# Kernel tuning notes

Hardware: AMD Instinct MI355X
Metric: run time of the kernel (lower is better)

Reference implementation:

```python
import jax, jax.numpy as jnp
import numpy as np

N_NODES = 50000
N_EDGES = 800000
D = 128
N_LAYERS = 5
N_REL = 500
N_ENT = 50000  # fc output size (num_entities)
BATCH = 1024


def setup_inputs() -> dict:
    key = jax.random.key(0)
    ks = jax.random.split(key, 10)
    return {
        "entity_embed": jax.random.normal(ks[0], (N_NODES, D), dtype=jnp.float32),
        "edge_val": jnp.ones((N_EDGES,), dtype=jnp.float32),
        "gnn_W": jax.random.normal(ks[1], (N_LAYERS, D, D), dtype=jnp.float32) * (1.0 / np.sqrt(D)),
        "gnn_b": jax.random.normal(ks[2], (N_LAYERS, D), dtype=jnp.float32) * 0.01,
        "rel_table": jax.random.normal(ks[3], (N_REL, D), dtype=jnp.float32),
        "fc_W": jax.random.normal(ks[4], (2 * D, N_ENT), dtype=jnp.float32) * (1.0 / np.sqrt(2 * D)),
        "fc_b": jax.random.normal(ks[5], (N_ENT,), dtype=jnp.float32) * 0.01,
        "edge_row": jax.random.randint(ks[6], (N_EDGES,), 0, N_NODES, dtype=jnp.int32),
        "edge_col": jax.random.randint(ks[7], (N_EDGES,), 0, N_NODES, dtype=jnp.int32),
        "head_idx": jax.random.randint(ks[8], (BATCH,), 0, N_NODES, dtype=jnp.int32),
        "rel_ids": jax.random.randint(ks[9], (BATCH,), 0, N_REL, dtype=jnp.int32),
    }


def reference(entity_embed, edge_val, gnn_W, gnn_b, rel_table, fc_W, fc_b,
              edge_row, edge_col, head_idx, rel_ids):
    n_nodes = entity_embed.shape[0]

    def layer(x, wb):
        W, b = wb
        # sparse.mm(adj, x): out[row] += val * x[col]
        msgs = edge_val[:, None] * x[edge_col]          # [E, D]
        agg = jax.ops.segment_sum(msgs, edge_row, num_segments=n_nodes)  # [N, D]
        return jax.nn.relu(agg @ W + b), None

    all_embed, _ = jax.lax.scan(layer, entity_embed, (gnn_W, gnn_b))

    head_embed = all_embed[head_idx]                    # [B, D]
    rel_embed = rel_table[rel_ids]                      # [B, D]
    embed = jnp.concatenate([head_embed, rel_embed], axis=1)  # [B, 2D]
    logits = embed @ fc_W + fc_b                        # [B, N_ENT]
    return logits
```

## Files before the change

kernel.cpp:

```cpp
#include <hip/hip_runtime.h>


#define N_NODES 50000
#define N_EDGES 800000
#define D 128
#define N_LAYERS 5
#define N_ENT 50000
#define BATCH 1024
#define KDIM 256
#define SCAN_BLOCKS ((N_NODES + 255) / 256)
#define FC_NT 128

typedef __attribute__((ext_vector_type(8))) __bf16 bf16x8;
typedef __attribute__((ext_vector_type(4))) float f32x4;
typedef __attribute__((ext_vector_type(8))) unsigned short u16x8;
typedef __attribute__((ext_vector_type(4))) unsigned short u16x4;

__device__ inline unsigned short f2bf(float x) {
  unsigned int u = __float_as_uint(x);
  unsigned int r = (u + 0x7FFFu + ((u >> 16) & 1u)) >> 16;
  return (unsigned short)r;
}
__device__ inline float bf2f(unsigned short b) {
  return __uint_as_float(((unsigned int)b) << 16);
}

__global__ void zero_i32(int* __restrict__ p, int n) {
  int i = blockIdx.x * blockDim.x + threadIdx.x;
  if (i < n) p[i] = 0;
}

__global__ void hist_kernel(const int* __restrict__ rows, int* __restrict__ counts) {
  int i = blockIdx.x * blockDim.x + threadIdx.x;
  int stride = gridDim.x * blockDim.x;
  for (; i < N_EDGES; i += stride) atomicAdd(&counts[rows[i]], 1);
}

__device__ inline int block_exscan256(int v, int* wsum, int* tot) {
  int t = threadIdx.x, lane = t & 63, wid = t >> 6;
  int s = v;
#pragma unroll
  for (int off = 1; off < 64; off <<= 1) {
    int u = __shfl_up(s, off, 64);
    if (lane >= off) s += u;
  }
  if (lane == 63) wsum[wid] = s;
  __syncthreads();
  if (t == 0) {
    int run = 0;
#pragma unroll
    for (int w = 0; w < 4; ++w) { int tmp = wsum[w]; wsum[w] = run; run += tmp; }
    wsum[4] = run;
  }
  __syncthreads();
  *tot = wsum[4];
  return wsum[wid] + s - v;
}

__global__ __launch_bounds__(256) void scan1_kernel(const int* __restrict__ counts,
                                                    int* __restrict__ row_ptr,
                                                    int* __restrict__ bsum) {
  __shared__ int wsum[5];
  int i = blockIdx.x * 256 + threadIdx.x;
  int v = (i < N_NODES) ? counts[i] : 0;
  int tot;
  int ex = block_exscan256(v, wsum, &tot);
  if (i < N_NODES) row_ptr[i] = ex;
  if (threadIdx.x == 0) bsum[blockIdx.x] = tot;
}

__global__ __launch_bounds__(256) void scan2_kernel(int* __restrict__ bsum) {
  __shared__ int wsum[5];
  int t = threadIdx.x;
  int v = (t < SCAN_BLOCKS) ? bsum[t] : 0;
  int tot;
  int ex = block_exscan256(v, wsum, &tot);
  if (t < SCAN_BLOCKS) bsum[t] = ex;
}

__global__ __launch_bounds__(256) void scan3_kernel(const int* __restrict__ counts,
                                                    const int* __restrict__ bsum,
                                                    int* __restrict__ row_ptr,
                                                    int* __restrict__ cursor) {
  int i = blockIdx.x * 256 + threadIdx.x;
  if (i >= N_NODES) return;
  int ex = row_ptr[i] + bsum[blockIdx.x];
  row_ptr[i] = ex;
  cursor[i] = ex;
  if (i == N_NODES - 1) row_ptr[N_NODES] = ex + counts[i];
}

__global__ void scatter_kernel(const int* __restrict__ rows, const int* __restrict__ cols,
                               const float* __restrict__ vals, int* __restrict__ cursor,
                               int* __restrict__ col_s, float* __restrict__ val_s) {
  int i = blockIdx.x * blockDim.x + threadIdx.x;
  int stride = gridDim.x * blockDim.x;
  for (; i < N_EDGES; i += stride) {
    int r = rows[i];
    int pos = atomicAdd(&cursor[r], 1);
    col_s[pos] = cols[i];
    val_s[pos] = vals[i];
  }
}

__global__ __launch_bounds__(256) void tobf16_kernel(const float* __restrict__ src,
                                                     unsigned short* __restrict__ dst,
                                                     int n8) {
  int i = blockIdx.x * blockDim.x + threadIdx.x;
  if (i >= n8) return;
  float4 a = *(const float4*)&src[i * 8];
  float4 b = *(const float4*)&src[i * 8 + 4];
  u16x8 o;
  o[0] = f2bf(a.x); o[1] = f2bf(a.y); o[2] = f2bf(a.z); o[3] = f2bf(a.w);
  o[4] = f2bf(b.x); o[5] = f2bf(b.y); o[6] = f2bf(b.z); o[7] = f2bf(b.w);
  *(u16x8*)&dst[i * 8] = o;
}

__global__ void wconv_kernel(const float* __restrict__ gW, unsigned short* __restrict__ Wt5) {
  int idx = blockIdx.x * 256 + threadIdx.x;
  if (idx >= N_LAYERS * D * D) return;
  int l = idx / (D * D);
  int rem = idx - l * D * D;
  int j = rem >> 7;
  int k = rem & 127;
  Wt5[idx] = f2bf(gW[l * D * D + k * D + j]);
}

__global__ __launch_bounds__(256) void layer_fused(const unsigned short* __restrict__ xb,
                                                   const int* __restrict__ row_ptr,
                                                   const int* __restrict__ cols,
                                                   const float* __restrict__ vals,
                                                   const unsigned short* __restrict__ Bt,
                                                   const float* __restrict__ bias,
                                                   unsigned short* __restrict__ yb) {
  __shared__ unsigned short atile[64 * D];
  int t = threadIdx.x, lane = t & 63, wave = t >> 6;
  int q = lane >> 4, l16 = lane & 15;
  int r0 = blockIdx.x * 64;
  char* ab = (char*)atile;

#pragma unroll
  for (int p = 0; p < 4; ++p) {
    int row_l = wave * 16 + p * 4 + q;
    int r = r0 + row_l;
    float acc[8] = {0.f, 0.f, 0.f, 0.f, 0.f, 0.f, 0.f, 0.f};
    if (r < N_NODES) {
      int e0 = row_ptr[r], e1 = row_ptr[r + 1];
      for (int base = e0; base < e1; base += 16) {
        int idx = base + l16;
        bool ok = idx < e1;
        int cl = ok ? cols[idx] : 0;
        float vl = ok ? vals[idx] : 0.f;
        int cnt = min(16, e1 - base);
        int j = 0;
        for (; j + 4 <= cnt; j += 4) {
          int c[4]; float v[4]; u16x8 xv[4];
#pragma unroll
          for (int u = 0; u < 4; ++u) {
            c[u] = __shfl(cl, q * 16 + j + u);
            v[u] = __shfl(vl, q * 16 + j + u);
          }
#pragma unroll
          for (int u = 0; u < 4; ++u) xv[u] = *(const u16x8*)&xb[c[u] * D + l16 * 8];
#pragma unroll
          for (int u = 0; u < 4; ++u)
#pragma unroll
            for (int dd = 0; dd < 8; ++dd) acc[dd] = fmaf(v[u], bf2f(xv[u][dd]), acc[dd]);
        }
        for (; j < cnt; ++j) {
          int c = __shfl(cl, q * 16 + j);
          float v = __shfl(vl, q * 16 + j);
          u16x8 xv0 = *(const u16x8*)&xb[c * D + l16 * 8];
#pragma unroll
          for (int dd = 0; dd < 8; ++dd) acc[dd] = fmaf(v, bf2f(xv0[dd]), acc[dd]);
        }
      }
    }
    u16x8 o;
#pragma unroll
    for (int dd = 0; dd < 8; ++dd) o[dd] = f2bf(acc[dd]);
    *(u16x8*)(ab + row_l * 256 + ((l16 ^ (row_l & 7)) << 4)) = o;
  }
  __syncthreads();

  int lq = lane >> 4;
  f32x4 acc2[4][2];
#pragma unroll
  for (int m = 0; m < 4; ++m) { acc2[m][0] = (f32x4){0,0,0,0}; acc2[m][1] = (f32x4){0,0,0,0}; }
#pragma unroll
  for (int kk = 0; kk < 4; ++kk) {
    bf16x8 wfr[2];
#pragma unroll
    for (int nt = 0; nt < 2; ++nt)
      wfr[nt] = *(const bf16x8*)&Bt[(wave * 32 + nt * 16 + l16) * D + kk * 32 + lq * 8];
#pragma unroll
    for (int m = 0; m < 4; ++m) {
      int row_l = m * 16 + l16;
      bf16x8 afr = *(const bf16x8*)(ab + row_l * 256 + ((((kk * 4 + lq) ^ (row_l & 7)) << 4)));
      acc2[m][0] = __builtin_amdgcn_mfma_f32_16x16x32_bf16(wfr[0], afr, acc2[m][0], 0, 0, 0);
      acc2[m][1] = __builtin_amdgcn_mfma_f32_16x16x32_bf16(wfr[1], afr, acc2[m][1], 0, 0, 0);
    }
  }
#pragma unroll
  for (int nt = 0; nt < 2; ++nt) {
    int jb = wave * 32 + nt * 16 + lq * 4;
    float4 bb = *(const float4*)&bias[jb];
#pragma unroll
    for (int m = 0; m < 4; ++m) {
      int r = r0 + m * 16 + l16;
      if (r < N_NODES) {
        u16x4 o;
        o[0] = f2bf(fmaxf(acc2[m][nt][0] + bb.x, 0.f));
        o[1] = f2bf(fmaxf(acc2[m][nt][1] + bb.y, 0.f));
        o[2] = f2bf(fmaxf(acc2[m][nt][2] + bb.z, 0.f));
        o[3] = f2bf(fmaxf(acc2[m][nt][3] + bb.w, 0.f));
        *(u16x4*)&yb[(size_t)r * D + jb] = o;
      }
    }
  }
}

__global__ __launch_bounds__(256) void wt_kernel(const float* __restrict__ fcW,
                                                 unsigned short* __restrict__ Wt) {
  int n = blockIdx.x * 256 + threadIdx.x;
  int k0 = blockIdx.y * 8;
  if (n >= N_ENT) return;
  u16x8 pk;
#pragma unroll
  for (int e = 0; e < 8; ++e) pk[e] = f2bf(fcW[(size_t)(k0 + e) * N_ENT + n]);
  *(u16x8*)&Wt[(size_t)n * KDIM + k0] = pk;
}

__global__ __launch_bounds__(256) void gather_bf16(const unsigned short* __restrict__ xb,
                                                   const float* __restrict__ rel_table,
                                                   const int* __restrict__ head_idx,
                                                   const int* __restrict__ rel_ids,
                                                   unsigned short* __restrict__ ebf) {
  int b = blockIdx.x;
  int k = threadIdx.x;
  unsigned short v;
  if (k < D) v = xb[head_idx[b] * D + k];
  else       v = f2bf(rel_table[rel_ids[b] * D + (k - D)]);
  ebf[b * KDIM + k] = v;
}

__global__ __launch_bounds__(256, 2) void fc_mfma(const unsigned short* __restrict__ ebf,
                                                  const unsigned short* __restrict__ Wt,
                                                  const float* __restrict__ fcb,
                                                  float* __restrict__ out) {
  __shared__ unsigned short etile[64 * KDIM];
  int t = threadIdx.x;
  int lane = t & 63, wave = t >> 6;
  int l16 = lane & 15, lq = lane >> 4;
  int n0 = blockIdx.x * FC_NT;
  char* eb = (char*)etile;

  bf16x8 afr[2][8];
#pragma unroll
  for (int nt = 0; nt < 2; ++nt) {
    const unsigned short* wp = Wt + (size_t)(n0 + wave * 32 + nt * 16 + l16) * KDIM + lq * 8;
#pragma unroll
    for (int kk = 0; kk < 8; ++kk) afr[nt][kk] = *(const bf16x8*)(wp + kk * 32);
  }

  int n_st[2]; float4 bv[2];
#pragma unroll
  for (int nt = 0; nt < 2; ++nt) {
    n_st[nt] = n0 + wave * 32 + nt * 16 + lq * 4;
    bv[nt] = make_float4(0.f, 0.f, 0.f, 0.f);
    if (n_st[nt] < N_ENT) bv[nt] = *(const float4*)&fcb[n_st[nt]];
  }

  for (int bc = 0; bc < 8; ++bc) {
    int b0 = blockIdx.y * 512 + bc * 64;
    const char* esrc = (const char*)(ebf + (size_t)b0 * KDIM);
#pragma unroll
    for (int it = 0; it < 8; ++it) {
      int c = it * 256 + t;
      int row = c >> 5;
      int ci = c & 31;
      float4 v = *(const float4*)(esrc + (size_t)c * 16);
      *(float4*)(eb + row * 512 + ((ci ^ ((row & 7) << 2)) << 4)) = v;
    }
    __syncthreads();

    f32x4 acc[2][4];
#pragma unroll
    for (int nt = 0; nt < 2; ++nt)
#pragma unroll
      for (int m = 0; m < 4; ++m) acc[nt][m] = (f32x4){0.f, 0.f, 0.f, 0.f};

#pragma unroll
    for (int m = 0; m < 4; ++m) {
      int row = m * 16 + l16;
#pragma unroll
      for (int kk = 0; kk < 8; ++kk) {
        bf16x8 bfr = *(const bf16x8*)(eb + row * 512 + ((((kk * 4 + lq) ^ ((row & 7) << 2)) << 4)));
        acc[0][m] = __builtin_amdgcn_mfma_f32_16x16x32_bf16(afr[0][kk], bfr, acc[0][m], 0, 0, 0);
        acc[1][m] = __builtin_amdgcn_mfma_f32_16x16x32_bf16(afr[1][kk], bfr, acc[1][m], 0, 0, 0);
      }
    }

#pragma unroll
    for (int nt = 0; nt < 2; ++nt) {
      if (n_st[nt] < N_ENT) {
#pragma unroll
        for (int m = 0; m < 4; ++m) {
          int b = b0 + m * 16 + l16;
          float4 o = {acc[nt][m][0] + bv[nt].x, acc[nt][m][1] + bv[nt].y,
                      acc[nt][m][2] + bv[nt].z, acc[nt][m][3] + bv[nt].w};
          *(float4*)&out[(size_t)b * N_ENT + n_st[nt]] = o;
        }
      }
    }
    __syncthreads();
  }
}

extern "C" void kernel_launch(void* const* d_in, const int* in_sizes, int n_in,
                              void* d_out, int out_size, void* d_ws, size_t ws_size,
                              hipStream_t stream) {
  const float* entity    = (const float*)d_in[0];
  const float* edge_val  = (const float*)d_in[1];
  const float* gnn_W     = (const float*)d_in[2];
  const float* gnn_b     = (const float*)d_in[3];
  const float* rel_table = (const float*)d_in[4];
  const float* fc_W      = (const float*)d_in[5];
  const float* fc_b      = (const float*)d_in[6];
  const int* edge_row    = (const int*)d_in[7];
  const int* edge_col    = (const int*)d_in[8];
  const int* head_idx    = (const int*)d_in[9];
  const int* rel_ids     = (const int*)d_in[10];
  float* out = (float*)d_out;

  char* ws = (char*)d_ws;
  size_t off = 0;
  auto alloc = [&](size_t bytes) -> void* {
    void* p = ws + off;
    off = (off + bytes + 255) & ~(size_t)255;
    return p;
  };
  int* counts   = (int*)alloc((size_t)N_NODES * 4);
  int* row_ptr  = (int*)alloc((size_t)(N_NODES + 1) * 4);
  int* cursor   = (int*)alloc((size_t)N_NODES * 4);
  int* bsum     = (int*)alloc((size_t)256 * 4);
  int* col_s    = (int*)alloc((size_t)N_EDGES * 4);
  float* val_s  = (float*)alloc((size_t)N_EDGES * 4);
  unsigned short* xA    = (unsigned short*)alloc((size_t)N_NODES * D * 2);
  unsigned short* xB    = (unsigned short*)alloc((size_t)N_NODES * D * 2);
  unsigned short* entbf = (unsigned short*)alloc((size_t)N_NODES * D * 2);
  unsigned short* ebf   = (unsigned short*)alloc((size_t)BATCH * KDIM * 2);
  unsigned short* Wt    = (unsigned short*)alloc((size_t)(N_ENT + 256) * KDIM * 2);
  unsigned short* Wt5   = (unsigned short*)alloc((size_t)N_LAYERS * D * D * 2);

  zero_i32<<<(N_NODES + 255) / 256, 256, 0, stream>>>(counts, N_NODES);
  hist_kernel<<<1024, 256, 0, stream>>>(edge_row, counts);
  scan1_kernel<<<SCAN_BLOCKS, 256, 0, stream>>>(counts, row_ptr, bsum);
  scan2_kernel<<<1, 256, 0, stream>>>(bsum);
  scan3_kernel<<<SCAN_BLOCKS, 256, 0, stream>>>(counts, bsum, row_ptr, cursor);
  scatter_kernel<<<1024, 256, 0, stream>>>(edge_row, edge_col, edge_val, cursor, col_s, val_s);

  tobf16_kernel<<<(N_NODES * D / 8 + 255) / 256, 256, 0, stream>>>(entity, entbf, N_NODES * D / 8);
  wconv_kernel<<<(N_LAYERS * D * D + 255) / 256, 256, 0, stream>>>(gnn_W, Wt5);

  for (int layer = 0; layer < N_LAYERS; ++layer) {
    const unsigned short* xin = (layer == 0) ? entbf : ((layer & 1) ? xA : xB);
    unsigned short* yout = (layer & 1) ? xB : xA;
    layer_fused<<<(N_NODES + 63) / 64, 256, 0, stream>>>(xin, row_ptr, col_s, val_s,
                                                         Wt5 + (size_t)layer * D * D,
                                                         gnn_b + (size_t)layer * D, yout);
  }

  dim3 wtg((N_ENT + 255) / 256, KDIM / 8);
  wt_kernel<<<wtg, 256, 0, stream>>>(fc_W, Wt);
  gather_bf16<<<BATCH, KDIM, 0, stream>>>(xA, rel_table, head_idx, rel_ids, ebf);

  dim3 fcg((N_ENT + FC_NT - 1) / FC_NT, 2);
  fc_mfma<<<fcg, 256, 0, stream>>>(ebf, Wt, fc_b, out);
}
```

Measured before the change: 401.2 us.

## Compute final GNN layer only for the batch's head nodes

The last message-passing layer now runs only on the 1024 head-index rows instead of all 50000 nodes. A new kernel aggregates neighbours and applies W+bias+ReLU for just those rows, writing straight into the FC input buffer. A separate kernel fills the relation half, replacing the old gather kernel. This removes about a fifth of the GNN aggregation work plus one full-graph layer launch. It relies on the output needing only the head rows, which holds for this model.

```diff
diff --git a/kernel.cpp b/kernel.cpp
--- a/kernel.cpp
+++ b/kernel.cpp
@@ -124,6 +124,32 @@
   int j = rem >> 7;
   int k = rem & 127;
   Wt5[idx] = f2bf(gW[l * D * D + k * D + j]);
+}
+
+__device__ inline void agg_batch(int cl, float vl, int cnt, int q, int l16,
+                                 const unsigned short* __restrict__ xb, float* acc) {
+  int j = 0;
+  for (; j + 4 <= cnt; j += 4) {
+    int c[4]; float v[4]; u16x8 xv[4];
+#pragma unroll
+    for (int u = 0; u < 4; ++u) {
+      c[u] = __shfl(cl, q * 16 + j + u);
+      v[u] = __shfl(vl, q * 16 + j + u);
+    }
+#pragma unroll
+    for (int u = 0; u < 4; ++u) xv[u] = *(const u16x8*)&xb[c[u] * D + l16 * 8];
+#pragma unroll
+    for (int u = 0; u < 4; ++u)
+#pragma unroll
+      for (int dd = 0; dd < 8; ++dd) acc[dd] = fmaf(v[u], bf2f(xv[u][dd]), acc[dd]);
+  }
+  for (; j < cnt; ++j) {
+    int c = __shfl(cl, q * 16 + j);
+    float v = __shfl(vl, q * 16 + j);
+    u16x8 xv0 = *(const u16x8*)&xb[c * D + l16 * 8];
+#pragma unroll
+    for (int dd = 0; dd < 8; ++dd) acc[dd] = fmaf(v, bf2f(xv0[dd]), acc[dd]);
+  }
 }
 
 __global__ __launch_bounds__(256) void layer_fused(const unsigned short* __restrict__ xb,
@@ -151,29 +177,7 @@
         bool ok = idx < e1;
         int cl = ok ? cols[idx] : 0;
         float vl = ok ? vals[idx] : 0.f;
-        int cnt = min(16, e1 - base);
-        int j = 0;
-        for (; j + 4 <= cnt; j += 4) {
-          int c[4]; float v[4]; u16x8 xv[4];
-#pragma unroll
-          for (int u = 0; u < 4; ++u) {
-            c[u] = __shfl(cl, q * 16 + j + u);
-            v[u] = __shfl(vl, q * 16 + j + u);
-          }
-#pragma unroll
-          for (int u = 0; u < 4; ++u) xv[u] = *(const u16x8*)&xb[c[u] * D + l16 * 8];
-#pragma unroll
-          for (int u = 0; u < 4; ++u)
-#pragma unroll
-            for (int dd = 0; dd < 8; ++dd) acc[dd] = fmaf(v[u], bf2f(xv[u][dd]), acc[dd]);
-        }
-        for (; j < cnt; ++j) {
-          int c = __shfl(cl, q * 16 + j);
-          float v = __shfl(vl, q * 16 + j);
-          u16x8 xv0 = *(const u16x8*)&xb[c * D + l16 * 8];
-#pragma unroll
-          for (int dd = 0; dd < 8; ++dd) acc[dd] = fmaf(v, bf2f(xv0[dd]), acc[dd]);
-        }
+        agg_batch(cl, vl, min(16, e1 - base), q, l16, xb, acc);
       }
     }
     u16x8 o;
@@ -220,6 +224,84 @@
   }
 }
 
+__global__ __launch_bounds__(256) void layer_head(const unsigned short* __restrict__ xb,
+                                                  const int* __restrict__ row_ptr,
+                                                  const int* __restrict__ cols,
+                                                  const float* __restrict__ vals,
+                                                  const int* __restrict__ head_idx,
+                                                  const unsigned short* __restrict__ Bt,
+                                                  const float* __restrict__ bias,
+                                                  unsigned short* __restrict__ ebf) {
+  __shared__ unsigned short atile[64 * D];
+  int t = threadIdx.x, lane = t & 63, wave = t >> 6;
+  int q = lane >> 4, l16 = lane & 15;
+  int r0 = blockIdx.x * 64;
+  char* ab = (char*)atile;
+
+#pragma unroll
+  for (int p = 0; p < 4; ++p) {
+    int row_l = wave * 16 + p * 4 + q;
+    int b = r0 + row_l;
+    int r = head_idx[b];
+    float acc[8] = {0.f, 0.f, 0.f, 0.f, 0.f, 0.f, 0.f, 0.f};
+    int e0 = row_ptr[r], e1 = row_ptr[r + 1];
+    for (int base = e0; base < e1; base += 16) {
+      int idx = base + l16;
+      bool ok = idx < e1;
+      int cl = ok ? cols[idx] : 0;
+      float vl = ok ? vals[idx] : 0.f;
+      agg_batch(cl, vl, min(16, e1 - base), q, l16, xb, acc);
+    }
+    u16x8 o;
+#pragma unroll
+    for (int dd = 0; dd < 8; ++dd) o[dd] = f2bf(acc[dd]);
+    *(u16x8*)(ab + row_l * 256 + ((l16 ^ (row_l & 7)) << 4)) = o;
+  }
+  __syncthreads();
+
+  int lq = lane >> 4;
+  f32x4 acc2[4][2];
+#pragma unroll
+  for (int m = 0; m < 4; ++m) { acc2[m][0] = (f32x4){0,0,0,0}; acc2[m][1] = (f32x4){0,0,0,0}; }
+#pragma unroll
+  for (int kk = 0; kk < 4; ++kk) {
+    bf16x8 wfr[2];
+#pragma unroll
+    for (int nt = 0; nt < 2; ++nt)
+      wfr[nt] = *(const bf16x8*)&Bt[(wave * 32 + nt * 16 + l16) * D + kk * 32 + lq * 8];
+#pragma unroll
+    for (int m = 0; m < 4; ++m) {
+      int row_l = m * 16 + l16;
+      bf16x8 afr = *(const bf16x8*)(ab + row_l * 256 + ((((kk * 4 + lq) ^ (row_l & 7)) << 4)));
+      acc2[m][0] = __builtin_amdgcn_mfma_f32_16x16x32_bf16(wfr[0], afr, acc2[m][0], 0, 0, 0);
+      acc2[m][1] = __builtin_amdgcn_mfma_f32_16x16x32_bf16(wfr[1], afr, acc2[m][1], 0, 0, 0);
+    }
+  }
+#pragma unroll
+  for (int nt = 0; nt < 2; ++nt) {
+    int jb = wave * 32 + nt * 16 + lq * 4;
+    float4 bb = *(const float4*)&bias[jb];
+#pragma unroll
+    for (int m = 0; m < 4; ++m) {
+      int b = r0 + m * 16 + l16;
+      u16x4 o;
+      o[0] = f2bf(fmaxf(acc2[m][nt][0] + bb.x, 0.f));
+      o[1] = f2bf(fmaxf(acc2[m][nt][1] + bb.y, 0.f));
+      o[2] = f2bf(fmaxf(acc2[m][nt][2] + bb.z, 0.f));
+      o[3] = f2bf(fmaxf(acc2[m][nt][3] + bb.w, 0.f));
+      *(u16x4*)&ebf[(size_t)b * KDIM + jb] = o;
+    }
+  }
+}
+
+__global__ __launch_bounds__(128) void rel_fill(const float* __restrict__ rel_table,
+                                                const int* __restrict__ rel_ids,
+                                                unsigned short* __restrict__ ebf) {
+  int b = blockIdx.x;
+  int k = threadIdx.x;
+  ebf[(size_t)b * KDIM + D + k] = f2bf(rel_table[rel_ids[b] * D + k]);
+}
+
 __global__ __launch_bounds__(256) void wt_kernel(const float* __restrict__ fcW,
                                                  unsigned short* __restrict__ Wt) {
   int n = blockIdx.x * 256 + threadIdx.x;
@@ -229,19 +311,6 @@
 #pragma unroll
   for (int e = 0; e < 8; ++e) pk[e] = f2bf(fcW[(size_t)(k0 + e) * N_ENT + n]);
   *(u16x8*)&Wt[(size_t)n * KDIM + k0] = pk;
-}
-
-__global__ __launch_bounds__(256) void gather_bf16(const unsigned short* __restrict__ xb,
-                                                   const float* __restrict__ rel_table,
-                                                   const int* __restrict__ head_idx,
-                                                   const int* __restrict__ rel_ids,
-                                                   unsigned short* __restrict__ ebf) {
-  int b = blockIdx.x;
-  int k = threadIdx.x;
-  unsigned short v;
-  if (k < D) v = xb[head_idx[b] * D + k];
-  else       v = f2bf(rel_table[rel_ids[b] * D + (k - D)]);
-  ebf[b * KDIM + k] = v;
 }
 
 __global__ __launch_bounds__(256, 2) void fc_mfma(const unsigned short* __restrict__ ebf,
@@ -363,7 +432,7 @@
   tobf16_kernel<<<(N_NODES * D / 8 + 255) / 256, 256, 0, stream>>>(entity, entbf, N_NODES * D / 8);
   wconv_kernel<<<(N_LAYERS * D * D + 255) / 256, 256, 0, stream>>>(gnn_W, Wt5);
 
-  for (int layer = 0; layer < N_LAYERS; ++layer) {
+  for (int layer = 0; layer < N_LAYERS - 1; ++layer) {
     const unsigned short* xin = (layer == 0) ? entbf : ((layer & 1) ? xA : xB);
     unsigned short* yout = (layer & 1) ? xB : xA;
     layer_fused<<<(N_NODES + 63) / 64, 256, 0, stream>>>(xin, row_ptr, col_s, val_s,
@@ -373,7 +442,11 @@
 
   dim3 wtg((N_ENT + 255) / 256, KDIM / 8);
   wt_kernel<<<wtg, 256, 0, stream>>>(fc_W, Wt);
-  gather_bf16<<<BATCH, KDIM, 0, stream>>>(xA, rel_table, head_idx, rel_ids, ebf);
+
+  layer_head<<<BATCH / 64, 256, 0, stream>>>(xB, row_ptr, col_s, val_s, head_idx,
+                                             Wt5 + (size_t)(N_LAYERS - 1) * D * D,
+                                             gnn_b + (size_t)(N_LAYERS - 1) * D, ebf);
+  rel_fill<<<BATCH, 128, 0, stream>>>(rel_table, rel_ids, ebf);
 
   dim3 fcg((N_ENT + FC_NT - 1) / FC_NT, 2);
   fc_mfma<<<fcg, 256, 0, stream>>>(ebf, Wt, fc_b, out);
```

New measurement: 385.2 us. 4.0% less time.
